# Kernel optimization log

Measured on AMD Instinct MI355X. Metric: run time of the kernel, lower is better.

## Reference

```python
import jax, jax.numpy as jnp
import numpy as np

V, E, NH, NL, FF, MAXLEN = 32000, 512, 8, 4, 2048, 80
B, L = 32, 80
EPS = 1e-5


def _ln(x, w, b):
    m = jnp.mean(x, axis=-1, keepdims=True)
    v = jnp.var(x, axis=-1, keepdims=True)
    return (x - m) / jnp.sqrt(v + EPS) * w + b


def _mha(q_in, kv_in, in_w, in_b, out_w, out_b, mask):
    # in_w: [3E, E] packed q/k/v like torch MultiheadAttention
    Bq, Lq, Em = q_in.shape
    Lk = kv_in.shape[1]
    hd = Em // NH
    q = q_in @ in_w[:Em].T + in_b[:Em]
    k = kv_in @ in_w[Em:2 * Em].T + in_b[Em:2 * Em]
    v = kv_in @ in_w[2 * Em:].T + in_b[2 * Em:]
    q = q.reshape(Bq, Lq, NH, hd).transpose(0, 2, 1, 3)
    k = k.reshape(Bq, Lk, NH, hd).transpose(0, 2, 1, 3)
    v = v.reshape(Bq, Lk, NH, hd).transpose(0, 2, 1, 3)
    s = jnp.einsum('bhqd,bhkd->bhqk', q, k) * (1.0 / float(np.sqrt(hd)))
    if mask is not None:
        s = s + mask
    a = jax.nn.softmax(s, axis=-1)
    o = jnp.einsum('bhqk,bhkd->bhqd', a, v).transpose(0, 2, 1, 3).reshape(Bq, Lq, Em)
    return o @ out_w.T + out_b


def _forward(caps, W_in, b_in, pos_emb, sa_in_w, sa_in_b, sa_out_w, sa_out_b,
             ca_in_w, ca_in_b, ca_out_w, ca_out_b, ff1_w, ff1_b, ff2_w, ff2_b,
             ln1_w, ln1_b, ln2_w, ln2_b, ln3_w, ln3_b, out_w, out_b):
    Bc, Lc = caps.shape
    # one-hot encode then dense Linear(vocab -> emb): semantically an embedding gather
    oh = jax.nn.one_hot(caps, V, dtype=jnp.float32)          # [B, L, V]
    x = oh @ W_in.T + b_in + pos_emb[:Lc][None]               # [B, L, E]
    mask = jnp.where(jnp.triu(jnp.ones((Lc, Lc), bool), 1), -jnp.inf, 0.0).astype(jnp.float32)
    mem = jnp.zeros((Bc, 1, E), jnp.float32)
    for i in range(NL):  # post-norm TransformerDecoderLayer (torch default, relu FFN)
        sa = _mha(x, x, sa_in_w[i], sa_in_b[i], sa_out_w[i], sa_out_b[i], mask)
        x = _ln(x + sa, ln1_w[i], ln1_b[i])
        ca = _mha(x, mem, ca_in_w[i], ca_in_b[i], ca_out_w[i], ca_out_b[i], None)
        x = _ln(x + ca, ln2_w[i], ln2_b[i])
        ff = jax.nn.relu(x @ ff1_w[i].T + ff1_b[i]) @ ff2_w[i].T + ff2_b[i]
        x = _ln(x + ff, ln3_w[i], ln3_b[i])
    return x @ out_w.T + out_b                                # [B, L, V]


def setup_inputs() -> dict:
    key = jax.random.key(0)
    ks = jax.random.split(key, 16)
    g = lambda k, shape, s=0.02: jax.random.normal(k, shape, jnp.float32) * s
    caps = jax.random.randint(ks[0], (B, L), 1, V)  # avoid pad_idx=0
    return {
        'caps': caps,
        'W_in': g(ks[1], (E, V)),
        'b_in': jnp.zeros((E,), jnp.float32),
        'pos_emb': g(ks[2], (MAXLEN, E)),
        'sa_in_w': g(ks[3], (NL, 3 * E, E)),
        'sa_in_b': jnp.zeros((NL, 3 * E), jnp.float32),
        'sa_out_w': g(ks[4], (NL, E, E)),
        'sa_out_b': jnp.zeros((NL, E), jnp.float32),
        'ca_in_w': g(ks[5], (NL, 3 * E, E)),
        'ca_in_b': jnp.zeros((NL, 3 * E), jnp.float32),
        'ca_out_w': g(ks[6], (NL, E, E)),
        'ca_out_b': jnp.zeros((NL, E), jnp.float32),
        'ff1_w': g(ks[7], (NL, FF, E)),
        'ff1_b': jnp.zeros((NL, FF), jnp.float32),
        'ff2_w': g(ks[8], (NL, E, FF)),
        'ff2_b': jnp.zeros((NL, E), jnp.float32),
        'ln1_w': jnp.ones((NL, E), jnp.float32),
        'ln1_b': jnp.zeros((NL, E), jnp.float32),
        'ln2_w': jnp.ones((NL, E), jnp.float32),
        'ln2_b': jnp.zeros((NL, E), jnp.float32),
        'ln3_w': jnp.ones((NL, E), jnp.float32),
        'ln3_b': jnp.zeros((NL, E), jnp.float32),
        'out_w': g(ks[9], (V, E)),
        'out_b': jnp.zeros((V,), jnp.float32),
    }


def reference(caps, W_in, b_in, pos_emb, sa_in_w, sa_in_b, sa_out_w, sa_out_b,
              ca_in_w, ca_in_b, ca_out_w, ca_out_b, ff1_w, ff1_b, ff2_w, ff2_b,
              ln1_w, ln1_b, ln2_w, ln2_b, ln3_w, ln3_b, out_w, out_b):
    return _forward(caps, W_in, b_in, pos_emb, sa_in_w, sa_in_b, sa_out_w, sa_out_b,
                    ca_in_w, ca_in_b, ca_out_w, ca_out_b, ff1_w, ff1_b, ff2_w, ff2_b,
                    ln1_w, ln1_b, ln2_w, ln2_b, ln3_w, ln3_b, out_w, out_b)
```

## Files before the change

### kernel.cpp

```cpp
#include <hip/hip_runtime.h>

typedef __attribute__((ext_vector_type(8))) short short8;
typedef __attribute__((ext_vector_type(4))) float floatx4;

__device__ __forceinline__ unsigned short f2bf(float f) {
  union { float f; unsigned int u; } un; un.f = f;
  unsigned int r = un.u + 0x7FFFu + ((un.u >> 16) & 1u);
  return (unsigned short)(r >> 16);
}
__device__ __forceinline__ float bf2f(unsigned short h) {
  union { unsigned int u; float f; } un; un.u = ((unsigned int)h) << 16;
  return un.f;
}

__device__ __forceinline__ void async_ld16(const unsigned short* g, unsigned short* l) {
  __builtin_amdgcn_global_load_lds(
      (const __attribute__((address_space(1))) void*)g,
      (__attribute__((address_space(3))) void*)l, 16, 0, 0);
}

__global__ __launch_bounds__(512, 1)
void gemm_vocab(const unsigned short* __restrict__ A, const unsigned short* __restrict__ B,
                const float* __restrict__ bias, float* __restrict__ C, int M, int N) {
  __shared__ __align__(16) unsigned short sB[65536];
  __shared__ __align__(16) unsigned short sA[2][4096];
  const int tid = threadIdx.x;
  const int lane = tid & 63;
  const int wave = tid >> 6;
  const int n0 = blockIdx.x * 128;
  const int fr = lane & 15;
  const int q = lane >> 4;
  const int wm = (wave >> 2) * 32;
  const int wn = (wave & 3) * 32;

  for (int ro = 0; ro < 16; ro++) {
    int rr = ro * 8 + wave;
    async_ld16(B + (size_t)(n0 + rr) * 512 + ((lane ^ (rr & 7)) << 3),
               &sB[ro * 4096 + wave * 512]);
  }

  auto stage_a = [&](int s, int buf) {
    int mt = s >> 3, kt = s & 7;
    int r = tid >> 3, cb = tid & 7;
    async_ld16(A + (size_t)(mt * 64 + r) * 512 + (kt << 6) + ((cb ^ (r & 7)) << 3),
               &sA[buf][wave * 512]);
  };

  floatx4 acc[2][2];
#pragma unroll
  for (int i = 0; i < 2; i++)
#pragma unroll
    for (int j = 0; j < 2; j++) acc[i][j] = (floatx4){0.f, 0.f, 0.f, 0.f};

  stage_a(0, 0);
  const int nsteps = (M >> 6) << 3;
  for (int s = 0; s < nsteps; s++) {
    __syncthreads();
    if (s + 1 < nsteps) stage_a(s + 1, (s + 1) & 1);
    const unsigned short* pA = sA[s & 1];
    const int kt = s & 7;
#pragma unroll
    for (int kk = 0; kk < 64; kk += 32) {
      const int cba = (kk >> 3) + q;
      short8 af[2], bfr[2];
#pragma unroll
      for (int t = 0; t < 2; t++) {
        int ra = wm + t * 16 + fr;
        af[t] = *(const short8*)&pA[ra * 64 + ((cba ^ (ra & 7)) << 3)];
        int rb = wn + t * 16 + fr;
        int cbi = (kt << 3) + cba;
        bfr[t] = *(const short8*)&sB[rb * 512 + ((cbi ^ (rb & 7)) << 3)];
      }
#pragma unroll
      for (int i = 0; i < 2; i++)
#pragma unroll
        for (int j = 0; j < 2; j++)
          acc[i][j] = __builtin_amdgcn_mfma_f32_16x16x32_bf16(af[i], bfr[j], acc[i][j], 0, 0, 0);
    }
    if (kt == 7) {
      const int mt = s >> 3;
#pragma unroll
      for (int i = 0; i < 2; i++)
#pragma unroll
        for (int j = 0; j < 2; j++) {
#pragma unroll
          for (int rg = 0; rg < 4; rg++) {
            int row = mt * 64 + wm + i * 16 + q * 4 + rg;
            int col = n0 + wn + j * 16 + fr;
            C[(size_t)row * N + col] = acc[i][j][rg] + bias[col];
          }
          acc[i][j] = (floatx4){0.f, 0.f, 0.f, 0.f};
        }
    }
  }
}

template<int TM, int TN, int OUT_BF16, int RELU>
__global__ __launch_bounds__(256, (TM == 64) ? 3 : 2)
void gemm_bt(const unsigned short* __restrict__ A, const unsigned short* __restrict__ B,
             const float* __restrict__ bias, const float* __restrict__ res,
             void* __restrict__ Cout, int M, int N, int K) {
  constexpr int AELEM = TM * 64;
  constexpr int BELEM = TN * 64;
  constexpr int AIT = AELEM / 2048;
  constexpr int BIT = BELEM / 2048;
  constexpr int LPS = AIT + BIT;
  constexpr int FM = TM / 32;
  constexpr int FN = TN / 32;
  __shared__ __align__(16) unsigned short sA[3][AELEM];
  __shared__ __align__(16) unsigned short sB[3][BELEM];
  const int tid = threadIdx.x;
  const int lane = tid & 63;
  const int wave = tid >> 6;

  const int gx = gridDim.x;
  const int nwg = gx * gridDim.y;
  const int ord = blockIdx.y * gx + blockIdx.x;
  const int qq = nwg >> 3, rr = nwg & 7;
  const int xcd = ord & 7, idx = ord >> 3;
  const int lin = (xcd < rr) ? (xcd * (qq + 1) + idx)
                             : (rr * (qq + 1) + (xcd - rr) * qq + idx);
  const int m0 = (lin % gx) * TM;
  const int n0 = (lin / gx) * TN;

  int a_off[AIT], b_off[BIT], lb[AIT > BIT ? AIT : BIT];
#pragma unroll
  for (int it = 0; it < AIT; it++) {
    int e = it * 2048 + tid * 8;
    int r = e >> 6, cb = (e >> 3) & 7;
    a_off[it] = (m0 + r) * K + ((cb ^ (r & 7)) * 8);
    lb[it] = it * 2048 + wave * 512;
  }
#pragma unroll
  for (int it = 0; it < BIT; it++) {
    int e = it * 2048 + tid * 8;
    int r = e >> 6, cb = (e >> 3) & 7;
    b_off[it] = (n0 + r) * K + ((cb ^ (r & 7)) * 8);
  }

  floatx4 acc[FM][FN];
#pragma unroll
  for (int i = 0; i < FM; i++)
#pragma unroll
    for (int j = 0; j < FN; j++) acc[i][j] = (floatx4){0.f, 0.f, 0.f, 0.f};

  const int nkt = K >> 6;
  const int wm = (wave >> 1) * (TM / 2);
  const int wn = (wave & 1) * (TN / 2);
  const int fr = lane & 15;
  const int q = lane >> 4;

  auto stage = [&](int kt, int buf) {
    const int k0 = kt << 6;
#pragma unroll
    for (int it = 0; it < AIT; it++) async_ld16(A + (size_t)a_off[it] + k0, &sA[buf][lb[it]]);
#pragma unroll
    for (int it = 0; it < BIT; it++) async_ld16(B + (size_t)b_off[it] + k0, &sB[buf][lb[it]]);
  };

  stage(0, 0);
  if (nkt > 1) stage(1, 1);
  if (nkt > 2) stage(2, 2);

  int buf = 0;
  for (int kt = 0; kt < nkt; kt++) {
    const int rem = nkt - 1 - kt;
    if (rem >= 2)      asm volatile("s_waitcnt vmcnt(%0)" :: "n"(2 * LPS) : "memory");
    else if (rem == 1) asm volatile("s_waitcnt vmcnt(%0)" :: "n"(LPS) : "memory");
    else               asm volatile("s_waitcnt vmcnt(0)" ::: "memory");
    __builtin_amdgcn_s_barrier();

    const unsigned short* pA = sA[buf];
    const unsigned short* pB = sB[buf];
#pragma unroll
    for (int kk = 0; kk < 64; kk += 32) {
      short8 af[FM], bfr[FN];
      const int cba = (kk >> 3) + q;
#pragma unroll
      for (int t = 0; t < FM; t++) {
        int ra = wm + t * 16 + fr;
        af[t] = *(const short8*)&pA[ra * 64 + ((cba ^ (ra & 7)) * 8)];
      }
#pragma unroll
      for (int t = 0; t < FN; t++) {
        int rb = wn + t * 16 + fr;
        bfr[t] = *(const short8*)&pB[rb * 64 + ((cba ^ (rb & 7)) * 8)];
      }
#pragma unroll
      for (int i = 0; i < FM; i++)
#pragma unroll
        for (int j = 0; j < FN; j++)
          acc[i][j] = __builtin_amdgcn_mfma_f32_16x16x32_bf16(af[i], bfr[j], acc[i][j], 0, 0, 0);
    }

    asm volatile("s_waitcnt lgkmcnt(0)" ::: "memory");
    __builtin_amdgcn_s_barrier();
    if (kt + 3 < nkt) stage(kt + 3, buf);
    buf = (buf == 2) ? 0 : buf + 1;
  }

#pragma unroll
  for (int i = 0; i < FM; i++) {
#pragma unroll
    for (int j = 0; j < FN; j++) {
#pragma unroll
      for (int rg = 0; rg < 4; rg++) {
        int row = m0 + wm + i * 16 + q * 4 + rg;
        int col = n0 + wn + j * 16 + fr;
        float v = acc[i][j][rg];
        if (bias) v += bias[col];
        if (res)  v += res[(size_t)row * N + col];
        if (RELU) v = v > 0.f ? v : 0.f;
        if (OUT_BF16) ((unsigned short*)Cout)[(size_t)row * N + col] = f2bf(v);
        else          ((float*)Cout)[(size_t)row * N + col] = v;
      }
    }
  }
}

__global__ __launch_bounds__(512)
void embed_kernel(const int* __restrict__ caps, const float* __restrict__ W_in,
                  const float* __restrict__ b_in, const float* __restrict__ pos,
                  float* __restrict__ x, unsigned short* __restrict__ xbf) {
  int pidx = blockIdx.x;
  int l = pidx % 80;
  int tok = caps[pidx];
  int e = threadIdx.x;
  float v = W_in[(size_t)e * 32000 + tok] + b_in[e] + pos[l * 512 + e];
  x[(size_t)pidx * 512 + e] = v;
  xbf[(size_t)pidx * 512 + e] = f2bf(v);
}

__global__ __launch_bounds__(256)
void ln_kernel(const float* __restrict__ in, const float* __restrict__ w,
               const float* __restrict__ b, float* __restrict__ xout,
               unsigned short* __restrict__ xbf) {
  int row = blockIdx.x * 4 + (threadIdx.x >> 6);
  int lane = threadIdx.x & 63;
  const float* p = in + (size_t)row * 512;
  float vals[8];
  float s = 0.f, s2 = 0.f;
#pragma unroll
  for (int j = 0; j < 8; j++) {
    float t = p[lane + j * 64];
    vals[j] = t; s += t; s2 += t * t;
  }
#pragma unroll
  for (int off = 32; off; off >>= 1) { s += __shfl_xor(s, off); s2 += __shfl_xor(s2, off); }
  float mean = s * (1.f / 512.f);
  float inv = rsqrtf(s2 * (1.f / 512.f) - mean * mean + 1e-5f);
#pragma unroll
  for (int j = 0; j < 8; j++) {
    int c = lane + j * 64;
    float y = (vals[j] - mean) * inv * w[c] + b[c];
    xout[(size_t)row * 512 + c] = y;
    xbf[(size_t)row * 512 + c] = f2bf(y);
  }
}

__global__ __launch_bounds__(256)
void ln2x_kernel(const float* __restrict__ in, const float* __restrict__ cav,
                 const float* __restrict__ w1, const float* __restrict__ b1,
                 const float* __restrict__ w2, const float* __restrict__ b2,
                 float* __restrict__ xout, unsigned short* __restrict__ xbf) {
  int row = blockIdx.x * 4 + (threadIdx.x >> 6);
  int lane = threadIdx.x & 63;
  const float* p = in + (size_t)row * 512;
  float vals[8];
  float s = 0.f, s2 = 0.f;
#pragma unroll
  for (int j = 0; j < 8; j++) {
    float t = p[lane + j * 64];
    vals[j] = t; s += t; s2 += t * t;
  }
#pragma unroll
  for (int off = 32; off; off >>= 1) { s += __shfl_xor(s, off); s2 += __shfl_xor(s2, off); }
  float mean = s * (1.f / 512.f);
  float inv = rsqrtf(s2 * (1.f / 512.f) - mean * mean + 1e-5f);
  float s_b = 0.f, s2_b = 0.f;
#pragma unroll
  for (int j = 0; j < 8; j++) {
    int c = lane + j * 64;
    float y = (vals[j] - mean) * inv * w1[c] + b1[c] + cav[c];
    vals[j] = y; s_b += y; s2_b += y * y;
  }
#pragma unroll
  for (int off = 32; off; off >>= 1) { s_b += __shfl_xor(s_b, off); s2_b += __shfl_xor(s2_b, off); }
  float mean2 = s_b * (1.f / 512.f);
  float inv2 = rsqrtf(s2_b * (1.f / 512.f) - mean2 * mean2 + 1e-5f);
#pragma unroll
  for (int j = 0; j < 8; j++) {
    int c = lane + j * 64;
    float y = (vals[j] - mean2) * inv2 * w2[c] + b2[c];
    xout[(size_t)row * 512 + c] = y;
    xbf[(size_t)row * 512 + c] = f2bf(y);
  }
}

__global__ __launch_bounds__(256)
void attn_kernel(const unsigned short* __restrict__ qkv, unsigned short* __restrict__ o) {
  __shared__ __align__(16) unsigned short sq[80][72];
  __shared__ __align__(16) unsigned short sk[80][72];
  __shared__ __align__(16) unsigned short svT[64][96];
  __shared__ __align__(16) unsigned short sp[80][96];
  __shared__ float ss[80][84];
  const int tid = threadIdx.x;
  const int lane = tid & 63;
  const int wave = tid >> 6;
  const int bb = blockIdx.x >> 3, hh = blockIdx.x & 7;
  const unsigned short* base = qkv + (size_t)bb * 80 * 1536 + hh * 64;

  for (int idx = tid; idx < 5120; idx += 256) {
    int r = idx >> 6, c = idx & 63;
    sq[r][c] = base[r * 1536 + c];
    sk[r][c] = base[r * 1536 + 512 + c];
    svT[c][r] = base[r * 1536 + 1024 + c];
  }
  for (int idx = tid; idx < 1024; idx += 256) svT[idx >> 4][80 + (idx & 15)] = 0;
  for (int idx = tid; idx < 1280; idx += 256) sp[idx >> 4][80 + (idx & 15)] = 0;
  __syncthreads();

  const int fr = lane & 15;
  const int q = lane >> 4;

  for (int t = wave; t < 25; t += 4) {
    int i0 = (t / 5) * 16, j0 = (t % 5) * 16;
    floatx4 acc = (floatx4){0.f, 0.f, 0.f, 0.f};
#pragma unroll
    for (int kk = 0; kk < 64; kk += 32) {
      short8 a = *(const short8*)&sq[i0 + fr][kk + q * 8];
      short8 b = *(const short8*)&sk[j0 + fr][kk + q * 8];
      acc = __builtin_amdgcn_mfma_f32_16x16x32_bf16(a, b, acc, 0, 0, 0);
    }
#pragma unroll
    for (int rg = 0; rg < 4; rg++) {
      int row = i0 + q * 4 + rg, col = j0 + fr;
      ss[row][col] = (col <= row) ? acc[rg] * 0.125f : -1e30f;
    }
  }
  __syncthreads();

  if (tid < 80) {
    float mx = -1e30f;
#pragma unroll
    for (int j = 0; j < 80; j++) mx = fmaxf(mx, ss[tid][j]);
    float sum = 0.f;
#pragma unroll
    for (int j = 0; j < 80; j++) { float e = __expf(ss[tid][j] - mx); ss[tid][j] = e; sum += e; }
    float inv = 1.f / sum;
#pragma unroll
    for (int j = 0; j < 80; j++) sp[tid][j] = f2bf(ss[tid][j] * inv);
  }
  __syncthreads();

  for (int t = wave; t < 20; t += 4) {
    int i0 = (t / 4) * 16, d0 = (t % 4) * 16;
    floatx4 acc = (floatx4){0.f, 0.f, 0.f, 0.f};
#pragma unroll
    for (int kk = 0; kk < 96; kk += 32) {
      short8 a = *(const short8*)&sp[i0 + fr][kk + q * 8];
      short8 b = *(const short8*)&svT[d0 + fr][kk + q * 8];
      acc = __builtin_amdgcn_mfma_f32_16x16x32_bf16(a, b, acc, 0, 0, 0);
    }
#pragma unroll
    for (int rg = 0; rg < 4; rg++) {
      int row = i0 + q * 4 + rg;
      o[((size_t)bb * 80 + row) * 512 + hh * 64 + d0 + fr] = f2bf(acc[rg]);
    }
  }
}

__global__ __launch_bounds__(256)
void cavec_kernel(const float* __restrict__ ca_out_w, const float* __restrict__ ca_in_b,
                  const float* __restrict__ ca_out_b, float* __restrict__ cav) {
  int g = blockIdx.x * 4 + (threadIdx.x >> 6);
  int lane = threadIdx.x & 63;
  int l = g >> 9, e = g & 511;
  const float* row = ca_out_w + ((size_t)l * 512 + e) * 512;
  const float* inb = ca_in_b + l * 1536 + 1024;
  float s = 0.f;
#pragma unroll
  for (int j = 0; j < 8; j++) s += row[lane + j * 64] * inb[lane + j * 64];
#pragma unroll
  for (int off = 32; off; off >>= 1) s += __shfl_xor(s, off);
  if (lane == 0) cav[g] = s + ca_out_b[l * 512 + e];
}

__global__ __launch_bounds__(256)
void convert_f2bf(const float* __restrict__ in, unsigned short* __restrict__ out, int n4) {
  int i = blockIdx.x * 256 + threadIdx.x;
  if (i < n4) {
    float4 v = ((const float4*)in)[i];
    ushort4 r;
    r.x = f2bf(v.x); r.y = f2bf(v.y); r.z = f2bf(v.z); r.w = f2bf(v.w);
    ((ushort4*)out)[i] = r;
  }
}

extern "C" void kernel_launch(void* const* d_in, const int* in_sizes, int n_in,
                              void* d_out, int out_size, void* d_ws, size_t ws_size,
                              hipStream_t stream) {
  const int*   caps     = (const int*)d_in[0];
  const float* W_in     = (const float*)d_in[1];
  const float* b_in     = (const float*)d_in[2];
  const float* pos_emb  = (const float*)d_in[3];
  const float* sa_in_w  = (const float*)d_in[4];
  const float* sa_in_b  = (const float*)d_in[5];
  const float* sa_out_w = (const float*)d_in[6];
  const float* sa_out_b = (const float*)d_in[7];
  const float* ca_in_b  = (const float*)d_in[9];
  const float* ca_out_w = (const float*)d_in[10];
  const float* ca_out_b = (const float*)d_in[11];
  const float* ff1_w    = (const float*)d_in[12];
  const float* ff1_b    = (const float*)d_in[13];
  const float* ff2_w    = (const float*)d_in[14];
  const float* ff2_b    = (const float*)d_in[15];
  const float* ln1_w    = (const float*)d_in[16];
  const float* ln1_b    = (const float*)d_in[17];
  const float* ln2_w    = (const float*)d_in[18];
  const float* ln2_b    = (const float*)d_in[19];
  const float* ln3_w    = (const float*)d_in[20];
  const float* ln3_b    = (const float*)d_in[21];
  const float* out_w    = (const float*)d_in[22];
  const float* out_b    = (const float*)d_in[23];

  char* ws = (char*)d_ws;
  size_t off = 0;
  auto alloc = [&](size_t bytes) {
    void* p = ws + off;
    off += (bytes + 255) & ~(size_t)255;
    return p;
  };
  unsigned short* w_sa_in  = (unsigned short*)alloc((size_t)4 * 1536 * 512 * 2);
  unsigned short* w_sa_out = (unsigned short*)alloc((size_t)4 * 512 * 512 * 2);
  unsigned short* w_ff1    = (unsigned short*)alloc((size_t)4 * 2048 * 512 * 2);
  unsigned short* w_ff2    = (unsigned short*)alloc((size_t)4 * 512 * 2048 * 2);
  unsigned short* w_out    = (unsigned short*)alloc((size_t)32000 * 512 * 2);
  float*          x        = (float*)alloc((size_t)2560 * 512 * 4);
  unsigned short* xbf      = (unsigned short*)alloc((size_t)2560 * 512 * 2);
  float*          t        = (float*)alloc((size_t)2560 * 512 * 4);
  unsigned short* qkv      = (unsigned short*)alloc((size_t)2560 * 1536 * 2);
  unsigned short* obf      = (unsigned short*)alloc((size_t)2560 * 512 * 2);
  unsigned short* hbf      = (unsigned short*)alloc((size_t)2560 * 2048 * 2);
  float*          cav      = (float*)alloc((size_t)2048 * 4);

  convert_f2bf<<<(786432 + 255) / 256, 256, 0, stream>>>(sa_in_w, w_sa_in, 786432);
  convert_f2bf<<<(262144 + 255) / 256, 256, 0, stream>>>(sa_out_w, w_sa_out, 262144);
  convert_f2bf<<<(1048576 + 255) / 256, 256, 0, stream>>>(ff1_w, w_ff1, 1048576);
  convert_f2bf<<<(1048576 + 255) / 256, 256, 0, stream>>>(ff2_w, w_ff2, 1048576);
  convert_f2bf<<<(4096000 + 255) / 256, 256, 0, stream>>>(out_w, w_out, 4096000);

  embed_kernel<<<2560, 512, 0, stream>>>(caps, W_in, b_in, pos_emb, x, xbf);
  cavec_kernel<<<512, 256, 0, stream>>>(ca_out_w, ca_in_b, ca_out_b, cav);

  for (int i = 0; i < 4; i++) {
    gemm_bt<128, 64, 1, 0><<<dim3(20, 24), 256, 0, stream>>>(
        xbf, w_sa_in + (size_t)i * 1536 * 512, sa_in_b + i * 1536, nullptr,
        qkv, 2560, 1536, 512);
    attn_kernel<<<256, 256, 0, stream>>>(qkv, obf);
    gemm_bt<64, 64, 0, 0><<<dim3(40, 8), 256, 0, stream>>>(
        obf, w_sa_out + (size_t)i * 512 * 512, sa_out_b + i * 512, x,
        t, 2560, 512, 512);
    ln2x_kernel<<<640, 256, 0, stream>>>(t, cav + i * 512,
        ln1_w + i * 512, ln1_b + i * 512, ln2_w + i * 512, ln2_b + i * 512, x, xbf);
    gemm_bt<128, 64, 1, 1><<<dim3(20, 32), 256, 0, stream>>>(
        xbf, w_ff1 + (size_t)i * 2048 * 512, ff1_b + i * 2048, nullptr,
        hbf, 2560, 2048, 512);
    gemm_bt<64, 64, 0, 0><<<dim3(40, 8), 256, 0, stream>>>(
        hbf, w_ff2 + (size_t)i * 512 * 2048, ff2_b + i * 512, x,
        t, 2560, 512, 2048);
    ln_kernel<<<640, 256, 0, stream>>>(t, ln3_w + i * 512, ln3_b + i * 512, x, xbf);
  }

  gemm_vocab<<<250, 512, 0, stream>>>(xbf, w_out, out_b, (float*)d_out, 2560, 32000);
}
```

Before: 1.122 ms.

## Convert vocab weights inside vocab GEMM, merge prep kernels, shrink residual GEMM tiles

The vocab GEMM now loads the fp32 output weights directly and rounds them to bf16 while staging into LDS. This drops the separate 32000x512 conversion pass and its intermediate bf16 buffer. The remaining weight conversions are merged into one launch, and the embedding and cross-attention-vector kernels are merged into another, to cut launch count. The two N=512 residual GEMMs switch to 32-row tiles with twice as many blocks to improve CU occupancy, at the cost of less weight reuse per block.

Result: faster. 1.070 ms (-4.6%).

```diff
diff --git a/kernel.cpp b/kernel.cpp
--- a/kernel.cpp
+++ b/kernel.cpp
@@ -8,10 +8,6 @@
   unsigned int r = un.u + 0x7FFFu + ((un.u >> 16) & 1u);
   return (unsigned short)(r >> 16);
 }
-__device__ __forceinline__ float bf2f(unsigned short h) {
-  union { unsigned int u; float f; } un; un.u = ((unsigned int)h) << 16;
-  return un.f;
-}
 
 __device__ __forceinline__ void async_ld16(const unsigned short* g, unsigned short* l) {
   __builtin_amdgcn_global_load_lds(
@@ -20,7 +16,7 @@
 }
 
 __global__ __launch_bounds__(512, 1)
-void gemm_vocab(const unsigned short* __restrict__ A, const unsigned short* __restrict__ B,
+void gemm_vocab(const unsigned short* __restrict__ A, const float* __restrict__ Bf,
                 const float* __restrict__ bias, float* __restrict__ C, int M, int N) {
   __shared__ __align__(16) unsigned short sB[65536];
   __shared__ __align__(16) unsigned short sA[2][4096];
@@ -35,8 +31,15 @@
 
   for (int ro = 0; ro < 16; ro++) {
     int rr = ro * 8 + wave;
-    async_ld16(B + (size_t)(n0 + rr) * 512 + ((lane ^ (rr & 7)) << 3),
-               &sB[ro * 4096 + wave * 512]);
+    const float* src = Bf + (size_t)(n0 + rr) * 512 + lane * 8;
+    float4 v0 = ((const float4*)src)[0];
+    float4 v1 = ((const float4*)src)[1];
+    short8 w;
+    w[0] = (short)f2bf(v0.x); w[1] = (short)f2bf(v0.y);
+    w[2] = (short)f2bf(v0.z); w[3] = (short)f2bf(v0.w);
+    w[4] = (short)f2bf(v1.x); w[5] = (short)f2bf(v1.y);
+    w[6] = (short)f2bf(v1.z); w[7] = (short)f2bf(v1.w);
+    *(short8*)&sB[rr * 512 + ((lane ^ (rr & 7)) << 3)] = w;
   }
 
   auto stage_a = [&](int s, int buf) {
@@ -96,7 +99,7 @@
 }
 
 template<int TM, int TN, int OUT_BF16, int RELU>
-__global__ __launch_bounds__(256, (TM == 64) ? 3 : 2)
+__global__ __launch_bounds__(256, (TM == 32) ? 4 : (TM == 64) ? 3 : 2)
 void gemm_bt(const unsigned short* __restrict__ A, const unsigned short* __restrict__ B,
              const float* __restrict__ bias, const float* __restrict__ res,
              void* __restrict__ Cout, int M, int N, int K) {
@@ -105,7 +108,8 @@
   constexpr int AIT = AELEM / 2048;
   constexpr int BIT = BELEM / 2048;
   constexpr int LPS = AIT + BIT;
-  constexpr int FM = TM / 32;
+  constexpr int LBN = (AIT > BIT) ? AIT : BIT;
+  constexpr int FM = (TM + 31) / 32;
   constexpr int FN = TN / 32;
   __shared__ __align__(16) unsigned short sA[3][AELEM];
   __shared__ __align__(16) unsigned short sB[3][BELEM];
@@ -123,13 +127,14 @@
   const int m0 = (lin % gx) * TM;
   const int n0 = (lin / gx) * TN;
 
-  int a_off[AIT], b_off[BIT], lb[AIT > BIT ? AIT : BIT];
+  int a_off[AIT], b_off[BIT], lb[LBN];
+#pragma unroll
+  for (int it = 0; it < LBN; it++) lb[it] = it * 2048 + wave * 512;
 #pragma unroll
   for (int it = 0; it < AIT; it++) {
     int e = it * 2048 + tid * 8;
     int r = e >> 6, cb = (e >> 3) & 7;
     a_off[it] = (m0 + r) * K + ((cb ^ (r & 7)) * 8);
-    lb[it] = it * 2048 + wave * 512;
   }
 #pragma unroll
   for (int it = 0; it < BIT; it++) {
@@ -219,16 +224,32 @@
 }
 
 __global__ __launch_bounds__(512)
-void embed_kernel(const int* __restrict__ caps, const float* __restrict__ W_in,
-                  const float* __restrict__ b_in, const float* __restrict__ pos,
-                  float* __restrict__ x, unsigned short* __restrict__ xbf) {
-  int pidx = blockIdx.x;
-  int l = pidx % 80;
-  int tok = caps[pidx];
-  int e = threadIdx.x;
-  float v = W_in[(size_t)e * 32000 + tok] + b_in[e] + pos[l * 512 + e];
-  x[(size_t)pidx * 512 + e] = v;
-  xbf[(size_t)pidx * 512 + e] = f2bf(v);
+void embed_cavec_kernel(const int* __restrict__ caps, const float* __restrict__ W_in,
+                        const float* __restrict__ b_in, const float* __restrict__ pos,
+                        float* __restrict__ x, unsigned short* __restrict__ xbf,
+                        const float* __restrict__ ca_out_w, const float* __restrict__ ca_in_b,
+                        const float* __restrict__ ca_out_b, float* __restrict__ cav) {
+  int bid = blockIdx.x;
+  if (bid < 2560) {
+    int l = bid % 80;
+    int tok = caps[bid];
+    int e = threadIdx.x;
+    float v = W_in[(size_t)e * 32000 + tok] + b_in[e] + pos[l * 512 + e];
+    x[(size_t)bid * 512 + e] = v;
+    xbf[(size_t)bid * 512 + e] = f2bf(v);
+  } else {
+    int wave = threadIdx.x >> 6, lane = threadIdx.x & 63;
+    int g = (bid - 2560) * 8 + wave;
+    int l = g >> 9, e = g & 511;
+    const float* row = ca_out_w + ((size_t)l * 512 + e) * 512;
+    const float* inb = ca_in_b + l * 1536 + 1024;
+    float s = 0.f;
+#pragma unroll
+    for (int j = 0; j < 8; j++) s += row[lane + j * 64] * inb[lane + j * 64];
+#pragma unroll
+    for (int off = 32; off; off >>= 1) s += __shfl_xor(s, off);
+    if (lane == 0) cav[g] = s + ca_out_b[l * 512 + e];
+  }
 }
 
 __global__ __launch_bounds__(256)
@@ -371,30 +392,20 @@
 }
 
 __global__ __launch_bounds__(256)
-void cavec_kernel(const float* __restrict__ ca_out_w, const float* __restrict__ ca_in_b,
-                  const float* __restrict__ ca_out_b, float* __restrict__ cav) {
-  int g = blockIdx.x * 4 + (threadIdx.x >> 6);
-  int lane = threadIdx.x & 63;
-  int l = g >> 9, e = g & 511;
-  const float* row = ca_out_w + ((size_t)l * 512 + e) * 512;
-  const float* inb = ca_in_b + l * 1536 + 1024;
-  float s = 0.f;
-#pragma unroll
-  for (int j = 0; j < 8; j++) s += row[lane + j * 64] * inb[lane + j * 64];
-#pragma unroll
-  for (int off = 32; off; off >>= 1) s += __shfl_xor(s, off);
-  if (lane == 0) cav[g] = s + ca_out_b[l * 512 + e];
-}
-
-__global__ __launch_bounds__(256)
-void convert_f2bf(const float* __restrict__ in, unsigned short* __restrict__ out, int n4) {
+void convert_all(const float* __restrict__ s0, unsigned short* __restrict__ d0,
+                 const float* __restrict__ s1, unsigned short* __restrict__ d1,
+                 const float* __restrict__ s2, unsigned short* __restrict__ d2,
+                 const float* __restrict__ s3, unsigned short* __restrict__ d3) {
   int i = blockIdx.x * 256 + threadIdx.x;
-  if (i < n4) {
-    float4 v = ((const float4*)in)[i];
-    ushort4 r;
-    r.x = f2bf(v.x); r.y = f2bf(v.y); r.z = f2bf(v.z); r.w = f2bf(v.w);
-    ((ushort4*)out)[i] = r;
-  }
+  const float* s; unsigned short* d; int j = i;
+  if (j < 786432) { s = s0; d = d0; }
+  else if ((j -= 786432) < 262144) { s = s1; d = d1; }
+  else if ((j -= 262144) < 1048576) { s = s2; d = d2; }
+  else { j -= 1048576; s = s3; d = d3; }
+  float4 v = ((const float4*)s)[j];
+  ushort4 r;
+  r.x = f2bf(v.x); r.y = f2bf(v.y); r.z = f2bf(v.z); r.w = f2bf(v.w);
+  ((ushort4*)d)[j] = r;
 }
 
 extern "C" void kernel_launch(void* const* d_in, const int* in_sizes, int n_in,
@@ -435,7 +446,6 @@
   unsigned short* w_sa_out = (unsigned short*)alloc((size_t)4 * 512 * 512 * 2);
   unsigned short* w_ff1    = (unsigned short*)alloc((size_t)4 * 2048 * 512 * 2);
   unsigned short* w_ff2    = (unsigned short*)alloc((size_t)4 * 512 * 2048 * 2);
-  unsigned short* w_out    = (unsigned short*)alloc((size_t)32000 * 512 * 2);
   float*          x        = (float*)alloc((size_t)2560 * 512 * 4);
   unsigned short* xbf      = (unsigned short*)alloc((size_t)2560 * 512 * 2);
   float*          t        = (float*)alloc((size_t)2560 * 512 * 4);
@@ -444,21 +454,17 @@
   unsigned short* hbf      = (unsigned short*)alloc((size_t)2560 * 2048 * 2);
   float*          cav      = (float*)alloc((size_t)2048 * 4);
 
-  convert_f2bf<<<(786432 + 255) / 256, 256, 0, stream>>>(sa_in_w, w_sa_in, 786432);
-  convert_f2bf<<<(262144 + 255) / 256, 256, 0, stream>>>(sa_out_w, w_sa_out, 262144);
-  convert_f2bf<<<(1048576 + 255) / 256, 256, 0, stream>>>(ff1_w, w_ff1, 1048576);
-  convert_f2bf<<<(1048576 + 255) / 256, 256, 0, stream>>>(ff2_w, w_ff2, 1048576);
-  convert_f2bf<<<(4096000 + 255) / 256, 256, 0, stream>>>(out_w, w_out, 4096000);
-
-  embed_kernel<<<2560, 512, 0, stream>>>(caps, W_in, b_in, pos_emb, x, xbf);
-  cavec_kernel<<<512, 256, 0, stream>>>(ca_out_w, ca_in_b, ca_out_b, cav);
+  convert_all<<<12288, 256, 0, stream>>>(sa_in_w, w_sa_in, sa_out_w, w_sa_out,
+                                         ff1_w, w_ff1, ff2_w, w_ff2);
+  embed_cavec_kernel<<<2816, 512, 0, stream>>>(caps, W_in, b_in, pos_emb, x, xbf,
+                                               ca_out_w, ca_in_b, ca_out_b, cav);
 
   for (int i = 0; i < 4; i++) {
     gemm_bt<128, 64, 1, 0><<<dim3(20, 24), 256, 0, stream>>>(
         xbf, w_sa_in + (size_t)i * 1536 * 512, sa_in_b + i * 1536, nullptr,
         qkv, 2560, 1536, 512);
     attn_kernel<<<256, 256, 0, stream>>>(qkv, obf);
-    gemm_bt<64, 64, 0, 0><<<dim3(40, 8), 256, 0, stream>>>(
+    gemm_bt<32, 64, 0, 0><<<dim3(80, 8), 256, 0, stream>>>(
         obf, w_sa_out + (size_t)i * 512 * 512, sa_out_b + i * 512, x,
         t, 2560, 512, 512);
     ln2x_kernel<<<640, 256, 0, stream>>>(t, cav + i * 512,
@@ -466,11 +472,11 @@
     gemm_bt<128, 64, 1, 1><<<dim3(20, 32), 256, 0, stream>>>(
         xbf, w_ff1 + (size_t)i * 2048 * 512, ff1_b + i * 2048, nullptr,
         hbf, 2560, 2048, 512);
-    gemm_bt<64, 64, 0, 0><<<dim3(40, 8), 256, 0, stream>>>(
+    gemm_bt<32, 64, 0, 0><<<dim3(80, 8), 256, 0, stream>>>(
         hbf, w_ff2 + (size_t)i * 512 * 2048, ff2_b + i * 512, x,
         t, 2560, 512, 2048);
     ln_kernel<<<640, 256, 0, stream>>>(t, ln3_w + i * 512, ln3_b + i * 512, x, xbf);
   }
 
-  gemm_vocab<<<250, 512, 0, stream>>>(xbf, w_out, out_b, (float*)d_out, 2560, 32000);
-}
+  gemm_vocab<<<250, 512, 0, stream>>>(xbf, out_w, out_b, (float*)d_out, 2560, 32000);
+}
```
